# Optimization experiments

Hardware: AMD Instinct MI355X
Metric: run time of the kernel (lower is better)

The kernel has to match this reference:

```python
import jax, jax.numpy as jnp
import numpy as np

B, L, DIM, HID, WIN = 1, 512, 64, 128, 4


def _ln(x, scale, bias, eps=1e-6):
    m = jnp.mean(x, axis=-1, keepdims=True)
    v = jnp.var(x, axis=-1, keepdims=True)
    return (x - m) / jnp.sqrt(v + eps) * scale + bias


def _banded_ingoing(left, right, w):
    # out[b,i,j,h] = sum_{k=i-w}^{i+w} left[b,k,i,h] * right[b,k,j,h]
    n = left.shape[1]
    ii = jnp.arange(n)
    offs = jnp.arange(-w, w + 1)
    rows = ii[:, None] + offs[None, :]                      # [L, 2w+1]
    valid = ((rows >= 0) & (rows < n)).astype(left.dtype)
    rows_c = jnp.clip(rows, 0, n - 1)
    # Lb[b,i,d,h] = left[b, i+d, i, h] (zero outside range)
    Lb = left[:, rows_c, ii[:, None], :] * valid[None, :, :, None]  # [B,L,2w+1,H]
    out = jnp.zeros_like(right)
    for di, dd in enumerate(range(-w, w + 1)):
        if dd >= 0:
            sh = jnp.pad(right[:, dd:], ((0, 0), (0, dd), (0, 0), (0, 0)))
        else:
            sh = jnp.pad(right[:, :dd], ((0, 0), (-dd, 0), (0, 0), (0, 0)))
        out = out + Lb[:, :, di, None, :] * sh
    return out


def setup_inputs() -> dict:
    key = jax.random.key(0)
    ks = jax.random.split(key, 8)
    d = {}
    d["x"] = jax.random.normal(ks[0], (B, L, L, DIM), dtype=jnp.float32)
    d["src_mask"] = jnp.ones((B, L), dtype=jnp.int32)
    d["norm_scale"] = jnp.ones((DIM,), jnp.float32)
    d["norm_bias"] = jnp.zeros((DIM,), jnp.float32)
    for i, nm in enumerate(["l", "r", "lg", "rg", "og"]):
        d[f"W{nm}"] = jax.random.normal(ks[i + 1], (DIM, HID), jnp.float32) * 0.02
        d[f"b{nm}"] = jnp.zeros((HID,), jnp.float32)
    d["out_norm_scale"] = jnp.ones((HID,), jnp.float32)
    d["out_norm_bias"] = jnp.zeros((HID,), jnp.float32)
    d["Wo"] = jax.random.normal(ks[6], (HID, DIM), jnp.float32) * 0.02
    d["bo"] = jnp.zeros((DIM,), jnp.float32)
    return d


def reference(x, src_mask, norm_scale, norm_bias, Wl, bl, Wr, br, Wlg, blg,
              Wrg, brg, Wog, bog, out_norm_scale, out_norm_bias, Wo, bo):
    m = src_mask.astype(jnp.float32)
    mask = (m[:, :, None] * m[:, None, :])[..., None]        # [B,L,L,1]
    xn = _ln(x, norm_scale, norm_bias)
    left = (xn @ Wl + bl) * mask * jax.nn.sigmoid(xn @ Wlg + blg)
    right = (xn @ Wr + br) * mask * jax.nn.sigmoid(xn @ Wrg + brg)
    out_gate = jax.nn.sigmoid(xn @ Wog + bog)
    out = _banded_ingoing(left, right, WIN)
    out = _ln(out, out_norm_scale, out_norm_bias) * out_gate
    return out @ Wo + bo
```

## Files before the change

### kernel.cpp

```cpp
#include <hip/hip_runtime.h>

typedef unsigned short u16;
typedef unsigned int u32;

#define LL 512
#define DIMC 64
#define HIDC 128

typedef __attribute__((ext_vector_type(8))) __bf16 bf16x8;
typedef __attribute__((ext_vector_type(4))) float f32x4;

__device__ __forceinline__ u16 f2bf(float f) {
  u32 u = __float_as_uint(f);
  u = u + 0x7FFFu + ((u >> 16) & 1u);
  return (u16)(u >> 16);
}
__device__ __forceinline__ float bf2f(u32 us) {
  return __uint_as_float(us << 16);
}
__device__ __forceinline__ float sigm(float x) {
  return 1.0f / (1.0f + __expf(-x));
}

extern "C" __global__ void prep(const float* __restrict__ Wr, const float* __restrict__ Wrg,
                                const float* __restrict__ Wog, const float* __restrict__ Wl,
                                const float* __restrict__ Wlg, const float* __restrict__ Wo,
                                u16* __restrict__ WTr, u16* __restrict__ WTl,
                                u16* __restrict__ WoT)
{
  int t = blockIdx.x * blockDim.x + threadIdx.x;
  int stride = gridDim.x * blockDim.x;
  for (int idx = t; idx < 384 * 64; idx += stride) {
    int n = idx >> 6, k = idx & 63;
    const float* W = (n < 128) ? Wr : (n < 256 ? Wrg : Wog);
    WTr[(n << 6) + (((k >> 3) ^ (n & 7)) << 3) + (k & 7)] = f2bf(W[k * HIDC + (n & 127)]);
  }
  for (int idx = t; idx < 256 * 64; idx += stride) {
    int n = idx >> 6, k = idx & 63;
    const float* W = (n < 128) ? Wl : Wlg;
    WTl[(n << 6) + (((k >> 3) ^ (n & 7)) << 3) + (k & 7)] = f2bf(W[k * HIDC + (n & 127)]);
  }
  for (int idx = t; idx < 64 * 128; idx += stride) {
    int d = idx >> 7, k = idx & 127;
    WoT[(d << 7) + (((k >> 3) ^ (d & 7)) << 3) + (k & 7)] = f2bf(Wo[k * DIMC + d]);
  }
}

extern "C" __global__ void __launch_bounds__(256, 2)
kernA(const float* __restrict__ x, const int* __restrict__ smask,
      const float* __restrict__ ns, const float* __restrict__ nb,
      const float* __restrict__ br, const float* __restrict__ brg,
      const float* __restrict__ bog, const u16* __restrict__ WTr,
      u16* __restrict__ ring, u16* og, int k0, int i0, int chunk)
{
  __shared__ u16 sWT[384 * 64];
  __shared__ u16 sA[64 * 64];
  const int bid = blockIdx.x;
  const int slot = bid >> 2, quarter = bid & 3;
  const int p = k0 + slot;
  if (p < 0 || p >= LL) return;
  const bool store_og = (p >= i0) && (p < i0 + chunk);
  const int t = threadIdx.x;
  const int lane = t & 63;
  const int wave = t >> 6;
  const int l15 = lane & 15, l4 = lane >> 4;

  {
    const uint4* src = (const uint4*)WTr;
    uint4* dst = (uint4*)sWT;
#pragma unroll
    for (int c = 0; c < 12; ++c) dst[t + c * 256] = src[t + c * 256];
  }

  const float mrow = (float)smask[p];
  const int ql = t >> 2, qc = t & 3;
  float4 nsv[4], nbv[4];
#pragma unroll
  for (int j = 0; j < 4; j++) {
    nsv[j] = *(const float4*)(ns + qc * 16 + j * 4);
    nbv[j] = *(const float4*)(nb + qc * 16 + j * 4);
  }
  float brv[2], brgv[2], bogv[2];
#pragma unroll
  for (int fp = 0; fp < 2; fp++) {
    int h = wave * 32 + fp * 16 + l15;
    brv[fp] = br[h]; brgv[fp] = brg[h]; bogv[fp] = bog[h];
  }

  for (int tile = quarter * 2; tile < quarter * 2 + 2; ++tile) {
    const int q0 = tile * 64;
    {
      const int q = q0 + ql;
      const float* xp = x + ((size_t)p * LL + q) * DIMC + qc * 16;
      float4 xv[4];
      float s = 0.f, ss = 0.f;
#pragma unroll
      for (int j = 0; j < 4; j++) {
        xv[j] = *(const float4*)(xp + j * 4);
        s += xv[j].x + xv[j].y + xv[j].z + xv[j].w;
        ss += xv[j].x * xv[j].x + xv[j].y * xv[j].y + xv[j].z * xv[j].z + xv[j].w * xv[j].w;
      }
      s += __shfl_xor(s, 1); ss += __shfl_xor(ss, 1);
      s += __shfl_xor(s, 2); ss += __shfl_xor(ss, 2);
      const float mean = s * (1.f / 64.f);
      const float var = ss * (1.f / 64.f) - mean * mean;
      const float rstd = rsqrtf(var + 1e-6f);
      u16 xb[16];
#pragma unroll
      for (int j = 0; j < 4; j++) {
        xb[j*4+0] = f2bf((xv[j].x - mean) * rstd * nsv[j].x + nbv[j].x);
        xb[j*4+1] = f2bf((xv[j].y - mean) * rstd * nsv[j].y + nbv[j].y);
        xb[j*4+2] = f2bf((xv[j].z - mean) * rstd * nsv[j].z + nbv[j].z);
        xb[j*4+3] = f2bf((xv[j].w - mean) * rstd * nsv[j].w + nbv[j].w);
      }
      uint4 c0, c1;
      c0.x = (u32)xb[0]  | ((u32)xb[1]  << 16);
      c0.y = (u32)xb[2]  | ((u32)xb[3]  << 16);
      c0.z = (u32)xb[4]  | ((u32)xb[5]  << 16);
      c0.w = (u32)xb[6]  | ((u32)xb[7]  << 16);
      c1.x = (u32)xb[8]  | ((u32)xb[9]  << 16);
      c1.y = (u32)xb[10] | ((u32)xb[11] << 16);
      c1.z = (u32)xb[12] | ((u32)xb[13] << 16);
      c1.w = (u32)xb[14] | ((u32)xb[15] << 16);
      char* rowp = (char*)sA + ql * 128;
      *(uint4*)(rowp + (((qc * 2 + 0) ^ (ql & 7)) << 4)) = c0;
      *(uint4*)(rowp + (((qc * 2 + 1) ^ (ql & 7)) << 4)) = c1;
    }
    __syncthreads();
    f32x4 acc[4][6];
    f32x4 zero = {0.f, 0.f, 0.f, 0.f};
#pragma unroll
    for (int m = 0; m < 4; m++)
#pragma unroll
      for (int f = 0; f < 6; f++) acc[m][f] = zero;
#pragma unroll
    for (int ks = 0; ks < 2; ks++) {
      bf16x8 av[4];
#pragma unroll
      for (int m = 0; m < 4; m++) {
        int row = m * 16 + l15;
        int ch = (ks * 4 + l4) ^ (row & 7);
        av[m] = *(const bf16x8*)((const char*)sA + row * 128 + (ch << 4));
      }
#pragma unroll
      for (int f = 0; f < 6; f++) {
        int g = f >> 1, fp = f & 1;
        int n = g * 128 + wave * 32 + fp * 16 + l15;
        int ch = (ks * 4 + l4) ^ (n & 7);
        bf16x8 bv = *(const bf16x8*)((const char*)sWT + n * 128 + (ch << 4));
#pragma unroll
        for (int m = 0; m < 4; m++)
          acc[m][f] = __builtin_amdgcn_mfma_f32_16x16x32_bf16(av[m], bv, acc[m][f], 0, 0, 0);
      }
    }
    __syncthreads();
#pragma unroll
    for (int m = 0; m < 4; m++) {
      float mv[4];
#pragma unroll
      for (int r = 0; r < 4; r++)
        mv[r] = mrow * (float)smask[q0 + m * 16 + l4 * 4 + r];
#pragma unroll
      for (int fp = 0; fp < 2; fp++) {
        const int h = wave * 32 + fp * 16 + l15;
        f32x4 lin = acc[m][fp];
        f32x4 gat = acc[m][2 + fp];
        f32x4 ogv = acc[m][4 + fp];
#pragma unroll
        for (int r = 0; r < 4; r++) {
          int qq = q0 + m * 16 + l4 * 4 + r;
          float rv = (lin[r] + brv[fp]) * mv[r] * sigm(gat[r] + brgv[fp]);
          ring[((size_t)slot * LL + qq) * HIDC + h] = f2bf(rv);
          if (store_og) {
            float ov = sigm(ogv[r] + bogv[fp]);
            og[((size_t)p * LL + qq) * HIDC + h] = f2bf(ov);
          }
        }
      }
    }
  }
}

extern "C" __global__ void __launch_bounds__(256, 2)
kernL(const float* __restrict__ x, const int* __restrict__ smask,
      const float* __restrict__ ns, const float* __restrict__ nb,
      const float* __restrict__ bl, const float* __restrict__ blg,
      const u16* __restrict__ WTl, float* __restrict__ Lbuf)
{
  __shared__ u16 sW[256 * 64];
  __shared__ u16 sA[64 * 64];
  const int g0 = blockIdx.x * 64;
  const int t = threadIdx.x;
  const int lane = t & 63, wave = t >> 6;
  const int l15 = lane & 15, l4 = lane >> 4;

  {
    const uint4* src = (const uint4*)WTl;
    uint4* dst = (uint4*)sW;
#pragma unroll
    for (int c = 0; c < 8; ++c) dst[t + c * 256] = src[t + c * 256];
  }

  const int ql = t >> 2, qc = t & 3;
  {
    const int g = g0 + ql;
    const int i = g / 9, d = g - 9 * i;
    int p = i + d - 4;
    p = (p < 0) ? 0 : (p > LL - 1 ? LL - 1 : p);
    const float* xp = x + ((size_t)p * LL + i) * DIMC + qc * 16;
    float4 xv[4];
    float s = 0.f, ss = 0.f;
#pragma unroll
    for (int j = 0; j < 4; j++) {
      xv[j] = *(const float4*)(xp + j * 4);
      s += xv[j].x + xv[j].y + xv[j].z + xv[j].w;
      ss += xv[j].x * xv[j].x + xv[j].y * xv[j].y + xv[j].z * xv[j].z + xv[j].w * xv[j].w;
    }
    s += __shfl_xor(s, 1); ss += __shfl_xor(ss, 1);
    s += __shfl_xor(s, 2); ss += __shfl_xor(ss, 2);
    const float mean = s * (1.f / 64.f);
    const float rstd = rsqrtf(ss * (1.f / 64.f) - mean * mean + 1e-6f);
    u16 xb[16];
#pragma unroll
    for (int j = 0; j < 4; j++) {
      const float4 nsv = *(const float4*)(ns + qc * 16 + j * 4);
      const float4 nbv = *(const float4*)(nb + qc * 16 + j * 4);
      xb[j*4+0] = f2bf((xv[j].x - mean) * rstd * nsv.x + nbv.x);
      xb[j*4+1] = f2bf((xv[j].y - mean) * rstd * nsv.y + nbv.y);
      xb[j*4+2] = f2bf((xv[j].z - mean) * rstd * nsv.z + nbv.z);
      xb[j*4+3] = f2bf((xv[j].w - mean) * rstd * nsv.w + nbv.w);
    }
    uint4 c0, c1;
    c0.x = (u32)xb[0]  | ((u32)xb[1]  << 16);
    c0.y = (u32)xb[2]  | ((u32)xb[3]  << 16);
    c0.z = (u32)xb[4]  | ((u32)xb[5]  << 16);
    c0.w = (u32)xb[6]  | ((u32)xb[7]  << 16);
    c1.x = (u32)xb[8]  | ((u32)xb[9]  << 16);
    c1.y = (u32)xb[10] | ((u32)xb[11] << 16);
    c1.z = (u32)xb[12] | ((u32)xb[13] << 16);
    c1.w = (u32)xb[14] | ((u32)xb[15] << 16);
    char* rowp = (char*)sA + ql * 128;
    *(uint4*)(rowp + (((qc * 2 + 0) ^ (ql & 7)) << 4)) = c0;
    *(uint4*)(rowp + (((qc * 2 + 1) ^ (ql & 7)) << 4)) = c1;
  }
  __syncthreads();
  f32x4 acc[4][4];
  f32x4 zero = {0.f, 0.f, 0.f, 0.f};
#pragma unroll
  for (int m = 0; m < 4; m++)
#pragma unroll
    for (int f = 0; f < 4; f++) acc[m][f] = zero;
#pragma unroll
  for (int ks = 0; ks < 2; ks++) {
    bf16x8 av[4];
#pragma unroll
    for (int m = 0; m < 4; m++) {
      int row = m * 16 + l15;
      int ch = (ks * 4 + l4) ^ (row & 7);
      av[m] = *(const bf16x8*)((const char*)sA + row * 128 + (ch << 4));
    }
#pragma unroll
    for (int f = 0; f < 4; f++) {
      int grp = f >> 1, fp = f & 1;
      int n = grp * 128 + wave * 32 + fp * 16 + l15;
      int ch = (ks * 4 + l4) ^ (n & 7);
      bf16x8 bv = *(const bf16x8*)((const char*)sW + n * 128 + (ch << 4));
#pragma unroll
      for (int m = 0; m < 4; m++)
        acc[m][f] = __builtin_amdgcn_mfma_f32_16x16x32_bf16(av[m], bv, acc[m][f], 0, 0, 0);
    }
  }
#pragma unroll
  for (int fp = 0; fp < 2; fp++) {
    const int h = wave * 32 + fp * 16 + l15;
    const float blv = bl[h], blgv = blg[h];
#pragma unroll
    for (int m = 0; m < 4; m++) {
      f32x4 lin = acc[m][fp];
      f32x4 gat = acc[m][2 + fp];
#pragma unroll
      for (int r = 0; r < 4; r++) {
        const int g = g0 + m * 16 + l4 * 4 + r;
        const int i = g / 9, d = g - 9 * i;
        const int p = i + d - 4;
        const bool valid = (p >= 0) && (p < LL);
        const float mv = valid ? (float)smask[i] * (float)smask[valid ? p : 0] : 0.f;
        Lbuf[(size_t)g * HIDC + h] = (lin[r] + blv) * mv * sigm(gat[r] + blgv);
      }
    }
  }
}

extern "C" __global__ void __launch_bounds__(256, 4)
kernB(const u16* __restrict__ ring, const u16* og,
      const float* __restrict__ Lbuf, const u16* __restrict__ WoT,
      const float* __restrict__ osc, const float* __restrict__ obi,
      const float* __restrict__ bo, float* out, int k0, int i0)
{
  __shared__ u16 sWo[64 * 128];
  __shared__ u16 sA[64 * 128];
  __shared__ float sLb[9 * 128];
  const int bid = blockIdx.x;
  const int i = i0 + (bid >> 3), j0 = (bid & 7) * 64;
  const int t = threadIdx.x;
  const int lane = t & 63, wave = t >> 6;
  const int l15 = lane & 15, l4 = lane >> 4;
  {
    const uint4* src = (const uint4*)WoT;
    uint4* dst = (uint4*)sWo;
#pragma unroll
    for (int c = 0; c < 4; ++c) dst[t + c * 256] = src[t + c * 256];
    const float* lb = Lbuf + (size_t)i * (9 * HIDC);
    for (int idx = t; idx < 9 * HIDC; idx += 256) sLb[idx] = lb[idx];
  }
  __syncthreads();
  const int j = t >> 2, hq = t & 3, h0 = hq * 32;
  float acc[32];
#pragma unroll
  for (int e = 0; e < 32; e++) acc[e] = 0.f;
  for (int d = 0; d < 9; d++) {
    const int k = i + d - 4;
    if (k < 0 || k >= LL) continue;
    const int slot = k - k0;
    const u16* rp = ring + ((size_t)slot * LL + j0 + j) * HIDC + h0;
#pragma unroll
    for (int c4 = 0; c4 < 4; c4++) {
      uint4 rv = *(const uint4*)(rp + c4 * 8);
      const float4 lb0 = *(const float4*)(sLb + d * 128 + h0 + c4 * 8);
      const float4 lb1 = *(const float4*)(sLb + d * 128 + h0 + c4 * 8 + 4);
      acc[c4*8+0] = fmaf(lb0.x, bf2f(rv.x & 0xffff), acc[c4*8+0]);
      acc[c4*8+1] = fmaf(lb0.y, bf2f(rv.x >> 16),    acc[c4*8+1]);
      acc[c4*8+2] = fmaf(lb0.z, bf2f(rv.y & 0xffff), acc[c4*8+2]);
      acc[c4*8+3] = fmaf(lb0.w, bf2f(rv.y >> 16),    acc[c4*8+3]);
      acc[c4*8+4] = fmaf(lb1.x, bf2f(rv.z & 0xffff), acc[c4*8+4]);
      acc[c4*8+5] = fmaf(lb1.y, bf2f(rv.z >> 16),    acc[c4*8+5]);
      acc[c4*8+6] = fmaf(lb1.z, bf2f(rv.w & 0xffff), acc[c4*8+6]);
      acc[c4*8+7] = fmaf(lb1.w, bf2f(rv.w >> 16),    acc[c4*8+7]);
    }
  }
  float s = 0.f, ss = 0.f;
#pragma unroll
  for (int e = 0; e < 32; e++) { s += acc[e]; ss += acc[e] * acc[e]; }
  s += __shfl_xor(s, 1); ss += __shfl_xor(ss, 1);
  s += __shfl_xor(s, 2); ss += __shfl_xor(ss, 2);
  const float mean = s * (1.f / 128.f);
  const float rstd = rsqrtf(ss * (1.f / 128.f) - mean * mean + 1e-6f);
  const u16* ogp = og + ((size_t)i * LL + j0 + j) * HIDC + h0;
  char* rowp = (char*)sA + j * 256;
#pragma unroll
  for (int c4 = 0; c4 < 4; c4++) {
    const float4 o0 = *(const float4*)(osc + h0 + c4 * 8);
    const float4 o1 = *(const float4*)(osc + h0 + c4 * 8 + 4);
    const float4 b0 = *(const float4*)(obi + h0 + c4 * 8);
    const float4 b1 = *(const float4*)(obi + h0 + c4 * 8 + 4);
    uint4 gv = *(const uint4*)(ogp + c4 * 8);
    float v0 = ((acc[c4*8+0] - mean) * rstd * o0.x + b0.x) * bf2f(gv.x & 0xffff);
    float v1 = ((acc[c4*8+1] - mean) * rstd * o0.y + b0.y) * bf2f(gv.x >> 16);
    float v2 = ((acc[c4*8+2] - mean) * rstd * o0.z + b0.z) * bf2f(gv.y & 0xffff);
    float v3 = ((acc[c4*8+3] - mean) * rstd * o0.w + b0.w) * bf2f(gv.y >> 16);
    float v4 = ((acc[c4*8+4] - mean) * rstd * o1.x + b1.x) * bf2f(gv.z & 0xffff);
    float v5 = ((acc[c4*8+5] - mean) * rstd * o1.y + b1.y) * bf2f(gv.z >> 16);
    float v6 = ((acc[c4*8+6] - mean) * rstd * o1.z + b1.z) * bf2f(gv.w & 0xffff);
    float v7 = ((acc[c4*8+7] - mean) * rstd * o1.w + b1.w) * bf2f(gv.w >> 16);
    uint4 pk;
    pk.x = (u32)f2bf(v0) | ((u32)f2bf(v1) << 16);
    pk.y = (u32)f2bf(v2) | ((u32)f2bf(v3) << 16);
    pk.z = (u32)f2bf(v4) | ((u32)f2bf(v5) << 16);
    pk.w = (u32)f2bf(v6) | ((u32)f2bf(v7) << 16);
    *(uint4*)(rowp + (((hq * 4 + c4) ^ (j & 7)) << 4)) = pk;
  }
  __syncthreads();
  f32x4 acc2[4];
  f32x4 zero = {0.f, 0.f, 0.f, 0.f};
#pragma unroll
  for (int m = 0; m < 4; m++) acc2[m] = zero;
#pragma unroll
  for (int ks = 0; ks < 4; ks++) {
    int n = wave * 16 + l15;
    int chb = (ks * 4 + l4) ^ (n & 7);
    bf16x8 bv = *(const bf16x8*)((const char*)sWo + n * 256 + (chb << 4));
#pragma unroll
    for (int m = 0; m < 4; m++) {
      int row = m * 16 + l15;
      int cha = (ks * 4 + l4) ^ (row & 7);
      bf16x8 av = *(const bf16x8*)((const char*)sA + row * 256 + (cha << 4));
      acc2[m] = __builtin_amdgcn_mfma_f32_16x16x32_bf16(av, bv, acc2[m], 0, 0, 0);
    }
  }
  const int dim = wave * 16 + l15;
  const float bov = bo[dim];
#pragma unroll
  for (int m = 0; m < 4; m++) {
#pragma unroll
    for (int r = 0; r < 4; r++) {
      int jj = j0 + m * 16 + l4 * 4 + r;
      out[((size_t)i * LL + jj) * DIMC + dim] = acc2[m][r] + bov;
    }
  }
}

extern "C" void kernel_launch(void* const* d_in, const int* in_sizes, int n_in,
                              void* d_out, int out_size, void* d_ws, size_t ws_size,
                              hipStream_t stream) {
  const float* x    = (const float*)d_in[0];
  const int*   sm   = (const int*)d_in[1];
  const float* ns   = (const float*)d_in[2];
  const float* nb   = (const float*)d_in[3];
  const float* Wl   = (const float*)d_in[4];
  const float* bl   = (const float*)d_in[5];
  const float* Wr   = (const float*)d_in[6];
  const float* br   = (const float*)d_in[7];
  const float* Wlg  = (const float*)d_in[8];
  const float* blg  = (const float*)d_in[9];
  const float* Wrg  = (const float*)d_in[10];
  const float* brg  = (const float*)d_in[11];
  const float* Wog  = (const float*)d_in[12];
  const float* bog  = (const float*)d_in[13];
  const float* osc  = (const float*)d_in[14];
  const float* obi  = (const float*)d_in[15];
  const float* Wo   = (const float*)d_in[16];
  const float* bo   = (const float*)d_in[17];

  const size_t LBUF_BYTES = (size_t)LL * 9 * HIDC * 4;
  char* ws = (char*)d_ws;
  float* Lbuf = (float*)ws;
  u16* WTr = (u16*)(ws + LBUF_BYTES);
  u16* WTl = (u16*)(ws + LBUF_BYTES + 49152);
  u16* WoT = (u16*)(ws + LBUF_BYTES + 49152 + 32768);
  u16* ring = (u16*)(ws + LBUF_BYTES + 49152 + 32768 + 16384);

  int CHUNK = 256;
  if (ws_size < LBUF_BYTES + 98304 + (size_t)(256 + 8) * LL * HIDC * 2) CHUNK = 64;
  u16* ogB = (u16*)d_out;

  prep<<<32, 256, 0, stream>>>(Wr, Wrg, Wog, Wl, Wlg, Wo, WTr, WTl, WoT);
  kernL<<<72, 256, 0, stream>>>(x, sm, ns, nb, bl, blg, WTl, Lbuf);
  for (int i0 = 0; i0 < LL; i0 += CHUNK) {
    const int k0 = i0 - 4;
    kernA<<<(CHUNK + 8) * 4, 256, 0, stream>>>(x, sm, ns, nb, br, brg, bog,
                                               WTr, ring, ogB, k0, i0, CHUNK);
    kernB<<<CHUNK * 8, 256, 0, stream>>>(ring, ogB, Lbuf, WoT, osc, obi, bo,
                                         (float*)d_out, k0, i0);
  }
}
```

Measured before the change: 178.6 us.

## Stage kernA outputs through LDS for coalesced stores and split tiles per block

kernA now processes a single 64-column tile per block, doubling the grid size. The gated right projection and output gate are written into a padded shared-memory tile and then copied to global memory with 16-byte coalesced stores. This replaces the scattered 2-byte per-element writes. In exchange, every block reloads the 48KB weight tile into LDS, that reload happens twice as often across the grid, and extra LDS and barriers are added.

```diff
diff --git a/kernel.cpp b/kernel.cpp
--- a/kernel.cpp
+++ b/kernel.cpp
@@ -55,8 +55,9 @@
 {
   __shared__ u16 sWT[384 * 64];
   __shared__ u16 sA[64 * 64];
+  __shared__ u16 sR[64 * 136];
   const int bid = blockIdx.x;
-  const int slot = bid >> 2, quarter = bid & 3;
+  const int slot = bid >> 3, tile = bid & 7;
   const int p = k0 + slot;
   if (p < 0 || p >= LL) return;
   const bool store_og = (p >= i0) && (p < i0 + chunk);
@@ -64,6 +65,7 @@
   const int lane = t & 63;
   const int wave = t >> 6;
   const int l15 = lane & 15, l4 = lane >> 4;
+  const int q0 = tile * 64;
 
   {
     const uint4* src = (const uint4*)WTr;
@@ -87,96 +89,121 @@
     brv[fp] = br[h]; brgv[fp] = brg[h]; bogv[fp] = bog[h];
   }
 
-  for (int tile = quarter * 2; tile < quarter * 2 + 2; ++tile) {
-    const int q0 = tile * 64;
-    {
-      const int q = q0 + ql;
-      const float* xp = x + ((size_t)p * LL + q) * DIMC + qc * 16;
-      float4 xv[4];
-      float s = 0.f, ss = 0.f;
-#pragma unroll
-      for (int j = 0; j < 4; j++) {
-        xv[j] = *(const float4*)(xp + j * 4);
-        s += xv[j].x + xv[j].y + xv[j].z + xv[j].w;
-        ss += xv[j].x * xv[j].x + xv[j].y * xv[j].y + xv[j].z * xv[j].z + xv[j].w * xv[j].w;
+  {
+    const int q = q0 + ql;
+    const float* xp = x + ((size_t)p * LL + q) * DIMC + qc * 16;
+    float4 xv[4];
+    float s = 0.f, ss = 0.f;
+#pragma unroll
+    for (int j = 0; j < 4; j++) {
+      xv[j] = *(const float4*)(xp + j * 4);
+      s += xv[j].x + xv[j].y + xv[j].z + xv[j].w;
+      ss += xv[j].x * xv[j].x + xv[j].y * xv[j].y + xv[j].z * xv[j].z + xv[j].w * xv[j].w;
+    }
+    s += __shfl_xor(s, 1); ss += __shfl_xor(ss, 1);
+    s += __shfl_xor(s, 2); ss += __shfl_xor(ss, 2);
+    const float mean = s * (1.f / 64.f);
+    const float var = ss * (1.f / 64.f) - mean * mean;
+    const float rstd = rsqrtf(var + 1e-6f);
+    u16 xb[16];
+#pragma unroll
+    for (int j = 0; j < 4; j++) {
+      xb[j*4+0] = f2bf((xv[j].x - mean) * rstd * nsv[j].x + nbv[j].x);
+      xb[j*4+1] = f2bf((xv[j].y - mean) * rstd * nsv[j].y + nbv[j].y);
+      xb[j*4+2] = f2bf((xv[j].z - mean) * rstd * nsv[j].z + nbv[j].z);
+      xb[j*4+3] = f2bf((xv[j].w - mean) * rstd * nsv[j].w + nbv[j].w);
+    }
+    uint4 c0, c1;
+    c0.x = (u32)xb[0]  | ((u32)xb[1]  << 16);
+    c0.y = (u32)xb[2]  | ((u32)xb[3]  << 16);
+    c0.z = (u32)xb[4]  | ((u32)xb[5]  << 16);
+    c0.w = (u32)xb[6]  | ((u32)xb[7]  << 16);
+    c1.x = (u32)xb[8]  | ((u32)xb[9]  << 16);
+    c1.y = (u32)xb[10] | ((u32)xb[11] << 16);
+    c1.z = (u32)xb[12] | ((u32)xb[13] << 16);
+    c1.w = (u32)xb[14] | ((u32)xb[15] << 16);
+    char* rowp = (char*)sA + ql * 128;
+    *(uint4*)(rowp + (((qc * 2 + 0) ^ (ql & 7)) << 4)) = c0;
+    *(uint4*)(rowp + (((qc * 2 + 1) ^ (ql & 7)) << 4)) = c1;
+  }
+  __syncthreads();
+  f32x4 acc[4][6];
+  f32x4 zero = {0.f, 0.f, 0.f, 0.f};
+#pragma unroll
+  for (int m = 0; m < 4; m++)
+#pragma unroll
+    for (int f = 0; f < 6; f++) acc[m][f] = zero;
+#pragma unroll
+  for (int ks = 0; ks < 2; ks++) {
+    bf16x8 av[4];
+#pragma unroll
+    for (int m = 0; m < 4; m++) {
+      int row = m * 16 + l15;
+      int ch = (ks * 4 + l4) ^ (row & 7);
+      av[m] = *(const bf16x8*)((const char*)sA + row * 128 + (ch << 4));
+    }
+#pragma unroll
+    for (int f = 0; f < 6; f++) {
+      int g = f >> 1, fp = f & 1;
+      int n = g * 128 + wave * 32 + fp * 16 + l15;
+      int ch = (ks * 4 + l4) ^ (n & 7);
+      bf16x8 bv = *(const bf16x8*)((const char*)sWT + n * 128 + (ch << 4));
+#pragma unroll
+      for (int m = 0; m < 4; m++)
+        acc[m][f] = __builtin_amdgcn_mfma_f32_16x16x32_bf16(av[m], bv, acc[m][f], 0, 0, 0);
+    }
+  }
+  float mv[4];
+#pragma unroll
+  for (int r = 0; r < 4; r++)
+    mv[r] = mrow;
+#pragma unroll
+  for (int m = 0; m < 4; m++) {
+    float mvr[4];
+#pragma unroll
+    for (int r = 0; r < 4; r++)
+      mvr[r] = mrow * (float)smask[q0 + m * 16 + l4 * 4 + r];
+#pragma unroll
+    for (int fp = 0; fp < 2; fp++) {
+      const int h = wave * 32 + fp * 16 + l15;
+      f32x4 lin = acc[m][fp];
+      f32x4 gat = acc[m][2 + fp];
+#pragma unroll
+      for (int r = 0; r < 4; r++) {
+        const int row = m * 16 + l4 * 4 + r;
+        sR[row * 136 + h] = f2bf((lin[r] + brv[fp]) * mvr[r] * sigm(gat[r] + brgv[fp]));
       }
-      s += __shfl_xor(s, 1); ss += __shfl_xor(ss, 1);
-      s += __shfl_xor(s, 2); ss += __shfl_xor(ss, 2);
-      const float mean = s * (1.f / 64.f);
-      const float var = ss * (1.f / 64.f) - mean * mean;
-      const float rstd = rsqrtf(var + 1e-6f);
-      u16 xb[16];
-#pragma unroll
-      for (int j = 0; j < 4; j++) {
-        xb[j*4+0] = f2bf((xv[j].x - mean) * rstd * nsv[j].x + nbv[j].x);
-        xb[j*4+1] = f2bf((xv[j].y - mean) * rstd * nsv[j].y + nbv[j].y);
-        xb[j*4+2] = f2bf((xv[j].z - mean) * rstd * nsv[j].z + nbv[j].z);
-        xb[j*4+3] = f2bf((xv[j].w - mean) * rstd * nsv[j].w + nbv[j].w);
-      }
-      uint4 c0, c1;
-      c0.x = (u32)xb[0]  | ((u32)xb[1]  << 16);
-      c0.y = (u32)xb[2]  | ((u32)xb[3]  << 16);
-      c0.z = (u32)xb[4]  | ((u32)xb[5]  << 16);
-      c0.w = (u32)xb[6]  | ((u32)xb[7]  << 16);
-      c1.x = (u32)xb[8]  | ((u32)xb[9]  << 16);
-      c1.y = (u32)xb[10] | ((u32)xb[11] << 16);
-      c1.z = (u32)xb[12] | ((u32)xb[13] << 16);
-      c1.w = (u32)xb[14] | ((u32)xb[15] << 16);
-      char* rowp = (char*)sA + ql * 128;
-      *(uint4*)(rowp + (((qc * 2 + 0) ^ (ql & 7)) << 4)) = c0;
-      *(uint4*)(rowp + (((qc * 2 + 1) ^ (ql & 7)) << 4)) = c1;
-    }
+    }
+  }
+  __syncthreads();
+  {
+    uint4* dst = (uint4*)(ring + ((size_t)slot * LL + q0) * HIDC);
+#pragma unroll
+    for (int c = 0; c < 4; c++) {
+      const int g = t + c * 256;
+      dst[g] = *(const uint4*)(sR + (g >> 4) * 136 + (g & 15) * 8);
+    }
+  }
+  if (store_og) {
     __syncthreads();
-    f32x4 acc[4][6];
-    f32x4 zero = {0.f, 0.f, 0.f, 0.f};
 #pragma unroll
     for (int m = 0; m < 4; m++)
-#pragma unroll
-      for (int f = 0; f < 6; f++) acc[m][f] = zero;
-#pragma unroll
-    for (int ks = 0; ks < 2; ks++) {
-      bf16x8 av[4];
-#pragma unroll
-      for (int m = 0; m < 4; m++) {
-        int row = m * 16 + l15;
-        int ch = (ks * 4 + l4) ^ (row & 7);
-        av[m] = *(const bf16x8*)((const char*)sA + row * 128 + (ch << 4));
-      }
-#pragma unroll
-      for (int f = 0; f < 6; f++) {
-        int g = f >> 1, fp = f & 1;
-        int n = g * 128 + wave * 32 + fp * 16 + l15;
-        int ch = (ks * 4 + l4) ^ (n & 7);
-        bf16x8 bv = *(const bf16x8*)((const char*)sWT + n * 128 + (ch << 4));
-#pragma unroll
-        for (int m = 0; m < 4; m++)
-          acc[m][f] = __builtin_amdgcn_mfma_f32_16x16x32_bf16(av[m], bv, acc[m][f], 0, 0, 0);
-      }
-    }
-    __syncthreads();
-#pragma unroll
-    for (int m = 0; m < 4; m++) {
-      float mv[4];
-#pragma unroll
-      for (int r = 0; r < 4; r++)
-        mv[r] = mrow * (float)smask[q0 + m * 16 + l4 * 4 + r];
 #pragma unroll
       for (int fp = 0; fp < 2; fp++) {
         const int h = wave * 32 + fp * 16 + l15;
-        f32x4 lin = acc[m][fp];
-        f32x4 gat = acc[m][2 + fp];
         f32x4 ogv = acc[m][4 + fp];
 #pragma unroll
         for (int r = 0; r < 4; r++) {
-          int qq = q0 + m * 16 + l4 * 4 + r;
-          float rv = (lin[r] + brv[fp]) * mv[r] * sigm(gat[r] + brgv[fp]);
-          ring[((size_t)slot * LL + qq) * HIDC + h] = f2bf(rv);
-          if (store_og) {
-            float ov = sigm(ogv[r] + bogv[fp]);
-            og[((size_t)p * LL + qq) * HIDC + h] = f2bf(ov);
-          }
+          const int row = m * 16 + l4 * 4 + r;
+          sR[row * 136 + h] = f2bf(sigm(ogv[r] + bogv[fp]));
         }
       }
+    __syncthreads();
+    uint4* dst = (uint4*)(og + ((size_t)p * LL + q0) * HIDC);
+#pragma unroll
+    for (int c = 0; c < 4; c++) {
+      const int g = t + c * 256;
+      dst[g] = *(const uint4*)(sR + (g >> 4) * 136 + (g & 15) * 8);
     }
   }
 }
@@ -437,7 +464,7 @@
   kernL<<<72, 256, 0, stream>>>(x, sm, ns, nb, bl, blg, WTl, Lbuf);
   for (int i0 = 0; i0 < LL; i0 += CHUNK) {
     const int k0 = i0 - 4;
-    kernA<<<(CHUNK + 8) * 4, 256, 0, stream>>>(x, sm, ns, nb, br, brg, bog,
+    kernA<<<(CHUNK + 8) * 8, 256, 0, stream>>>(x, sm, ns, nb, br, brg, bog,
                                                WTr, ring, ogB, k0, i0, CHUNK);
     kernB<<<CHUNK * 8, 256, 0, stream>>>(ring, ogB, Lbuf, WoT, osc, obi, bo,
                                          (float*)d_out, k0, i0);
```

Result: no change. 175.7 us (-1.6%).
